# Kernel optimization log

Measured on AMD Instinct MI355X. Metric: run time of the kernel, lower is better.

The kernel has to match this reference:

```python
import jax, jax.numpy as jnp
import numpy as np

N_HEADS = 8


def setup_inputs() -> dict:
    key = jax.random.key(0)
    ks = jax.random.split(key, 12)
    B, C, H, W = 16, 256, 64, 64
    std = 1.0 / np.sqrt(C)  # init_std(conv) ~ 1/sqrt(fan_in) for a 1x1 conv
    return {
        "x": jax.random.normal(ks[0], (B, C, H, W), jnp.float32),
        "mod_multiplier": jax.random.normal(ks[1], (B, C), jnp.float32),
        "mod_bias": jax.random.normal(ks[2], (B, C), jnp.float32),
        "qkv_w": jax.random.normal(ks[3], (3 * C, C), jnp.float32) * std,
        "qkv_b": jnp.zeros((3 * C,), jnp.float32),
        "pe_q_h": jax.random.normal(ks[4], (1, C, H, 1), jnp.float32) * 0.02,
        "pe_q_w": jax.random.normal(ks[5], (1, C, 1, W), jnp.float32) * 0.02,
        "pe_k_h": jax.random.normal(ks[6], (1, C, H, 1), jnp.float32) * 0.02,
        "pe_k_w": jax.random.normal(ks[7], (1, C, 1, W), jnp.float32) * 0.02,
        "pre_act_bias": jnp.zeros((1, C, 1, 1), jnp.float32),
        "pre_qkv_bias": jnp.zeros((1, C, 1, 1), jnp.float32),
    }


def reference(x, mod_multiplier, mod_bias, qkv_w, qkv_b, pe_q_h, pe_q_w, pe_k_h, pe_k_w, pre_act_bias, pre_qkv_bias):
    B, C, H, W = x.shape
    hs = C // N_HEADS  # head_size
    dot_scale = jnp.asarray(hs, x.dtype) ** 0.5

    x_preact = jax.nn.silu(x + pre_act_bias)
    # 1x1 conv == channel GEMM: [B,C,H,W] x [3C,C] -> [B,3C,H,W]
    qkv = jnp.einsum('bchw,oc->bohw', x_preact + pre_qkv_bias, qkv_w) + qkv_b[None, :, None, None]
    q, k, v = jnp.split(qkv, 3, axis=1)

    q = q + pe_q_h + pe_q_w
    k = k + pe_k_h + pe_k_w
    q = q * mod_multiplier[:, :, None, None] + mod_bias[:, :, None, None]

    # view as [B, n_heads, head_size, H*W]
    q = q.reshape(B, N_HEADS, hs, H * W)
    k = k.reshape(B, N_HEADS, hs, H * W)
    v = v.reshape(B, N_HEADS, hs, H * W)

    # channel-attention: logits [B, n_heads, hs, hs]
    logits = jnp.einsum('bhcn,bhdn->bhcd', q, k) / dot_scale
    weights = jax.nn.softmax(logits, axis=-1)
    out = jnp.einsum('bhcd,bhdn->bhcn', weights, v).reshape(B, C, H, W)

    return jnp.concatenate((x_preact, out), axis=1)
```

## Files before the change

kernel.cpp:

```cpp
#include <hip/hip_runtime.h>

typedef short bf16x8 __attribute__((ext_vector_type(8)));
typedef float f32x4 __attribute__((ext_vector_type(4)));

__device__ __forceinline__ float b2f(unsigned short u) {
  union { unsigned int i; float f; } v; v.i = ((unsigned int)u) << 16; return v.f;
}
__device__ __forceinline__ unsigned short f2b(float f) {
  unsigned int u = __float_as_uint(f);
  u += 0x7fffu + ((u >> 16) & 1u);
  return (unsigned short)(u >> 16);
}
__device__ __forceinline__ float silu_f(float s) { return s / (1.0f + __expf(-s)); }

__device__ __forceinline__ void split2(float f, unsigned short& h, unsigned short& l) {
  h = f2b(f);
  l = f2b(f - b2f(h));
}

__device__ __forceinline__ void gload16(const unsigned short* g, unsigned short* l) {
  __builtin_amdgcn_global_load_lds(
      (const __attribute__((address_space(1))) unsigned int*)g,
      (__attribute__((address_space(3))) unsigned int*)l, 16, 0, 0);
}

__device__ __forceinline__ void unpack8(const unsigned* p, bf16x8& hi, bf16x8& lo) {
  uint4 a = *(const uint4*)p;
  uint4 b = *(const uint4*)(p + 4);
  unsigned u[8] = {a.x, a.y, a.z, a.w, b.x, b.y, b.z, b.w};
  unsigned hw[4], lw[4];
  #pragma unroll
  for (int j = 0; j < 4; j++) {
    hw[j] = __builtin_amdgcn_perm(u[2 * j + 1], u[2 * j], 0x05040100u);
    lw[j] = __builtin_amdgcn_perm(u[2 * j + 1], u[2 * j], 0x07060302u);
  }
  hi = *(bf16x8*)hw;
  lo = *(bf16x8*)lw;
}

__global__ __launch_bounds__(256) void k_prep(
    const float* __restrict__ x, const float* __restrict__ pab,
    const float* __restrict__ pqb, const float* __restrict__ W,
    unsigned short* __restrict__ Wfq, unsigned short* __restrict__ Wfl,
    unsigned short* __restrict__ Wfv, float* __restrict__ out) {
  __shared__ unsigned th2[64 * 32], tl2[64 * 32];
  int blk = blockIdx.x;
  if (blk < 96) {
    int u = blk * 256 + threadIdx.x;
    int lane = u & 63, l15 = lane & 15, l4 = lane >> 4;
    int row, k;
    unsigned short* dh;
    unsigned short* dl = nullptr;
    if (u < 16384) {
      int i = (u >> 6) & 3, step = (u >> 8) & 7, hh = u >> 11;
      row = (i < 2) ? (hh * 32 + i * 16 + l15) : (256 + hh * 32 + (i - 2) * 16 + l15);
      k = step * 32 + l4 * 8;
      dh = Wfq + (long long)u * 8;
      dl = Wfl + (long long)u * 8;
    } else {
      int u2 = u - 16384;
      int i2 = (u2 >> 6) & 1, step = (u2 >> 7) & 7, hh = u2 >> 10;
      row = 512 + hh * 32 + i2 * 16 + l15;
      k = step * 32 + l4 * 8;
      dh = Wfv + (long long)u2 * 8;
    }
    float4 a = *(const float4*)(W + row * 256 + k);
    float4 bq = *(const float4*)(W + row * 256 + k + 4);
    float v[8] = {a.x, a.y, a.z, a.w, bq.x, bq.y, bq.z, bq.w};
    unsigned short h8[8], l8[8];
    #pragma unroll
    for (int j = 0; j < 8; j++) split2(v[j], h8[j], l8[j]);
    uint4 ph;
    ph.x = h8[0] | ((unsigned)h8[1] << 16); ph.y = h8[2] | ((unsigned)h8[3] << 16);
    ph.z = h8[4] | ((unsigned)h8[5] << 16); ph.w = h8[6] | ((unsigned)h8[7] << 16);
    *(uint4*)dh = ph;
    if (dl) {
      uint4 pl;
      pl.x = l8[0] | ((unsigned)l8[1] << 16); pl.y = l8[2] | ((unsigned)l8[3] << 16);
      pl.z = l8[4] | ((unsigned)l8[5] << 16); pl.w = l8[6] | ((unsigned)l8[7] << 16);
      *(uint4*)dl = pl;
    }
    return;
  }
  blk -= 96;
  int nb = blk & 63;
  int cb = (blk >> 6) & 3;
  int b = blk >> 8;
  int n0 = nb * 64, c0 = cb * 64;
  int t = threadIdx.x;
  int nn = (t & 15) * 4;
  #pragma unroll
  for (int p = 0; p < 2; p++) {
    int cp = p * 16 + (t >> 4);
    int c = 2 * cp;
    float pa0 = pab[c0 + c], pq0 = pqb[c0 + c];
    float pa1 = pab[c0 + c + 1], pq1 = pqb[c0 + c + 1];
    float4 x0 = *(const float4*)(x + ((long long)(b * 256 + c0 + c)) * 4096 + n0 + nn);
    float4 x1 = *(const float4*)(x + ((long long)(b * 256 + c0 + c + 1)) * 4096 + n0 + nn);
    float s0[4] = {silu_f(x0.x + pa0), silu_f(x0.y + pa0),
                   silu_f(x0.z + pa0), silu_f(x0.w + pa0)};
    float s1[4] = {silu_f(x1.x + pa1), silu_f(x1.y + pa1),
                   silu_f(x1.z + pa1), silu_f(x1.w + pa1)};
    float4 sv0 = {s0[0], s0[1], s0[2], s0[3]};
    float4 sv1 = {s1[0], s1[1], s1[2], s1[3]};
    *(float4*)(out + ((long long)(b * 512 + c0 + c)) * 4096 + n0 + nn) = sv0;
    *(float4*)(out + ((long long)(b * 512 + c0 + c + 1)) * 4096 + n0 + nn) = sv1;
    float t0[4] = {s0[0] + pq0, s0[1] + pq0, s0[2] + pq0, s0[3] + pq0};
    float t1[4] = {s1[0] + pq1, s1[1] + pq1, s1[2] + pq1, s1[3] + pq1};
    #pragma unroll
    for (int j = 0; j < 4; j++) {
      int nr = nn + j;
      unsigned short h0, l0, h1, l1;
      split2(t0[j], h0, l0);
      split2(t1[j], h1, l1);
      int pidx = nr * 32 + (cp ^ (nr & 31));
      th2[pidx] = (unsigned)h0 | ((unsigned)h1 << 16);
      tl2[pidx] = (unsigned)l0 | ((unsigned)l1 << 16);
    }
  }
  __syncthreads();
  unsigned short* Th = (unsigned short*)(out + ((long long)(b * 512 + 256)) * 4096);
  unsigned short* Tl = Th + 4096 * 256;
  #pragma unroll
  for (int q = 0; q < 2; q++) {
    int s = q * 256 + t;
    int n = s >> 3, sc = s & 7;
    unsigned wh[4], wl[4];
    #pragma unroll
    for (int j = 0; j < 4; j++) {
      int pidx = n * 32 + ((sc * 4 + j) ^ (n & 31));
      wh[j] = th2[pidx];
      wl[j] = tl2[pidx];
    }
    uint4 vh = {wh[0], wh[1], wh[2], wh[3]};
    uint4 vl = {wl[0], wl[1], wl[2], wl[3]};
    *(uint4*)(Th + (long long)(n0 + n) * 256 + c0 + sc * 8) = vh;
    *(uint4*)(Tl + (long long)(n0 + n) * 256 + c0 + sc * 8) = vl;
  }
}

__global__ __launch_bounds__(256, 3) void k_qkl(
    const unsigned short* __restrict__ Wfq, const unsigned short* __restrict__ Wfl,
    const unsigned short* __restrict__ Wfv,
    const float* __restrict__ qkvb,
    const float* __restrict__ peqh, const float* __restrict__ peqw,
    const float* __restrict__ pekh, const float* __restrict__ pekw,
    const float* __restrict__ modm, const float* __restrict__ modb,
    const float* __restrict__ outT, float* __restrict__ kv,
    float* __restrict__ logits) {
  __shared__ __align__(16) unsigned char smem[33792];
  unsigned short* stg = (unsigned short*)smem;
  unsigned* qk = (unsigned*)smem;
  float* red = (float*)smem;

  int bx = blockIdx.x;
  int ntile = bx & 31, h = (bx >> 5) & 7, b = bx >> 8;
  int n0 = ntile * 128;
  int t = threadIdx.x, lane = t & 63, w = t >> 6;
  int l15 = lane & 15, l4 = lane >> 4;

  const unsigned short* Th =
      (const unsigned short*)(outT + ((long long)(b * 512 + 256)) * 4096);
  const unsigned short* Tl = Th + 4096 * 256;

  const unsigned short* csrc[4];
  unsigned short* cdst[4];
  int lrow = lane >> 2;
  int lslot = ((lane & 3) ^ ((lane >> 3) & 3)) * 8;
  #pragma unroll
  for (int i = 0; i < 4; i++) {
    int c = w + 4 * i;
    const unsigned short* plane = (c < 8) ? Th : Tl;
    int rowb = n0 + (c & 7) * 16;
    csrc[i] = plane + (long long)(rowb + lrow) * 256 + lslot;
    cdst[i] = stg + c * 512;
  }

  const unsigned short* aqb = Wfq + (long long)(h * 32) * 512 + lane * 8;
  const unsigned short* alb = Wfl + (long long)(h * 32) * 512 + lane * 8;
  const unsigned short* avb = Wfv + (long long)(h * 16) * 512 + lane * 8;

  int sw = (l4 ^ ((l15 >> 1) & 3)) << 3;
  f32x4 z = {0.f, 0.f, 0.f, 0.f};
  f32x4 acc[4][2];
  f32x4 accv[2][2];
  #pragma unroll
  for (int i = 0; i < 4; i++)
    #pragma unroll
    for (int j = 0; j < 2; j++) acc[i][j] = z;
  #pragma unroll
  for (int i = 0; i < 2; i++)
    #pragma unroll
    for (int j = 0; j < 2; j++) accv[i][j] = z;

  for (int step = 0; step < 8; ++step) {
    int k0 = step * 32;
    #pragma unroll
    for (int i = 0; i < 4; i++) gload16(csrc[i] + k0, cdst[i]);
    bf16x8 ah[4], alo[4], av[2];
    #pragma unroll
    for (int i = 0; i < 4; i++) {
      ah[i]  = *(const bf16x8*)(aqb + (step * 4 + i) * 512);
      alo[i] = *(const bf16x8*)(alb + (step * 4 + i) * 512);
    }
    #pragma unroll
    for (int i = 0; i < 2; i++)
      av[i] = *(const bf16x8*)(avb + (step * 2 + i) * 512);
    __syncthreads();
    bf16x8 bh[2], bl[2];
    #pragma unroll
    for (int j = 0; j < 2; j++) {
      int ro = (w * 32 + j * 16 + l15) * 32 + sw;
      bh[j] = *(const bf16x8*)(stg + ro);
      bl[j] = *(const bf16x8*)(stg + 4096 + ro);
    }
    #pragma unroll
    for (int i = 0; i < 2; i++)
      #pragma unroll
      for (int j = 0; j < 2; j++)
        accv[i][j] = __builtin_amdgcn_mfma_f32_16x16x32_bf16(av[i], bh[j], accv[i][j], 0, 0, 0);
    #pragma unroll
    for (int i = 0; i < 4; i++)
      #pragma unroll
      for (int j = 0; j < 2; j++) {
        acc[i][j] = __builtin_amdgcn_mfma_f32_16x16x32_bf16(ah[i], bh[j], acc[i][j], 0, 0, 0);
        acc[i][j] = __builtin_amdgcn_mfma_f32_16x16x32_bf16(ah[i], bl[j], acc[i][j], 0, 0, 0);
        acc[i][j] = __builtin_amdgcn_mfma_f32_16x16x32_bf16(alo[i], bh[j], acc[i][j], 0, 0, 0);
      }
    __syncthreads();
  }

  int b256 = b * 256;
  #pragma unroll
  for (int i = 0; i < 2; i++) {
    #pragma unroll
    for (int r = 0; r < 4; r++) {
      int row = i * 16 + l4 * 4 + r;
      int cch = h * 32 + row;
      float bias = qkvb[512 + cch];
      #pragma unroll
      for (int j = 0; j < 2; j++) {
        int n = n0 + w * 32 + j * 16 + l15;
        kv[((long long)(b256 + cch)) * 4096 + n] = accv[i][j][r] + bias;
      }
    }
  }

  #pragma unroll
  for (int i = 0; i < 4; i++) {
    #pragma unroll
    for (int r = 0; r < 4; r++) {
      int row = i * 16 + l4 * 4 + r;
      int cch = h * 32 + (row & 31);
      float bias = qkvb[(row & 32) ? (256 + cch) : cch];
      float mm = 0.f, mb = 0.f;
      if (row < 32) { mm = modm[b256 + cch]; mb = modb[b256 + cch]; }
      #pragma unroll
      for (int j = 0; j < 2; j++) {
        int nl = w * 32 + j * 16 + l15;
        int n = n0 + nl;
        int hh = n >> 6, ww = n & 63;
        float v = acc[i][j][r] + bias;
        if (row < 32) {
          v += peqh[cch * 64 + hh] + peqw[cch * 64 + ww];
          v = v * mm + mb;
        } else {
          v += pekh[cch * 64 + hh] + pekw[cch * 64 + ww];
        }
        unsigned short hi_, lo_;
        split2(v, hi_, lo_);
        int pch = (nl >> 3) ^ (row & 15);
        qk[row * 132 + pch * 8 + (nl & 7)] = (unsigned)hi_ | ((unsigned)lo_ << 16);
      }
    }
  }
  __syncthreads();

  f32x4 acc2[2][2] = {z, z, z, z};
  int chn = w * 4 + l4;
  bf16x8 qh[2], ql[2], kh[2], kl[2];
  #pragma unroll
  for (int i2 = 0; i2 < 2; i2++) {
    int row = i2 * 16 + l15;
    unpack8(qk + row * 132 + ((chn ^ l15) << 3), qh[i2], ql[i2]);
    unpack8(qk + (row + 32) * 132 + ((chn ^ l15) << 3), kh[i2], kl[i2]);
  }
  acc2[0][0] = __builtin_amdgcn_mfma_f32_16x16x32_bf16(qh[0], kh[0], acc2[0][0], 0, 0, 0);
  acc2[0][0] = __builtin_amdgcn_mfma_f32_16x16x32_bf16(qh[0], kl[0], acc2[0][0], 0, 0, 0);
  acc2[0][0] = __builtin_amdgcn_mfma_f32_16x16x32_bf16(ql[0], kh[0], acc2[0][0], 0, 0, 0);
  acc2[0][1] = __builtin_amdgcn_mfma_f32_16x16x32_bf16(qh[0], kh[1], acc2[0][1], 0, 0, 0);
  acc2[0][1] = __builtin_amdgcn_mfma_f32_16x16x32_bf16(qh[0], kl[1], acc2[0][1], 0, 0, 0);
  acc2[0][1] = __builtin_amdgcn_mfma_f32_16x16x32_bf16(ql[0], kh[1], acc2[0][1], 0, 0, 0);
  acc2[1][0] = __builtin_amdgcn_mfma_f32_16x16x32_bf16(qh[1], kh[0], acc2[1][0], 0, 0, 0);
  acc2[1][0] = __builtin_amdgcn_mfma_f32_16x16x32_bf16(qh[1], kl[0], acc2[1][0], 0, 0, 0);
  acc2[1][0] = __builtin_amdgcn_mfma_f32_16x16x32_bf16(ql[1], kh[0], acc2[1][0], 0, 0, 0);
  acc2[1][1] = __builtin_amdgcn_mfma_f32_16x16x32_bf16(qh[1], kh[1], acc2[1][1], 0, 0, 0);
  acc2[1][1] = __builtin_amdgcn_mfma_f32_16x16x32_bf16(qh[1], kl[1], acc2[1][1], 0, 0, 0);
  acc2[1][1] = __builtin_amdgcn_mfma_f32_16x16x32_bf16(ql[1], kh[1], acc2[1][1], 0, 0, 0);

  __syncthreads();
  #pragma unroll
  for (int i2 = 0; i2 < 2; i2++)
    #pragma unroll
    for (int j2 = 0; j2 < 2; j2++)
      #pragma unroll
      for (int r = 0; r < 4; r++)
        red[w * 1056 + (i2 * 16 + l4 * 4 + r) * 33 + j2 * 16 + l15] = acc2[i2][j2][r];
  __syncthreads();
  const float scale = 0.1767766952966369f;
  int bhid = b * 8 + h;
  #pragma unroll
  for (int i = 0; i < 4; i++) {
    int idx = i * 256 + t;
    int crow = idx >> 5, dcol = idx & 31;
    int ro = crow * 33 + dcol;
    float s = (red[ro] + red[1056 + ro] + red[2112 + ro] + red[3168 + ro]) * scale;
    atomicAdd(logits + (long long)bhid * 1024 + idx, s);
  }
}

__global__ __launch_bounds__(256) void k_pv(
    const float* __restrict__ kv,
    const float* __restrict__ logits,
    float* __restrict__ out) {
  int bx = blockIdx.x;
  int ntile = bx & 15, bh = bx >> 4;
  int b = bh >> 3, h = bh & 7;
  int t = threadIdx.x;
  __shared__ float raw[32][33];
  __shared__ float wsm[32][33];
  #pragma unroll
  for (int i = 0; i < 4; i++) {
    int idx = i * 256 + t;
    raw[idx >> 5][idx & 31] = logits[(long long)bh * 1024 + idx];
  }
  __syncthreads();
  if (t < 32) {
    float mx = -1e30f;
    for (int d = 0; d < 32; d++) mx = fmaxf(mx, raw[t][d]);
    float e[32]; float s = 0.f;
    for (int d = 0; d < 32; d++) { e[d] = __expf(raw[t][d] - mx); s += e[d]; }
    float inv = 1.0f / s;
    for (int d = 0; d < 32; d++) wsm[t][d] = e[d] * inv;
  }
  __syncthreads();
  int rg = t >> 6;
  int nl = (t & 63) * 4;
  int n0 = ntile * 256 + nl;
  const float* vb = kv + ((long long)(b * 256 + h * 32)) * 4096 + n0;
  float acc[8][4];
  #pragma unroll
  for (int r = 0; r < 8; r++)
    #pragma unroll
    for (int i = 0; i < 4; i++) acc[r][i] = 0.f;
  for (int d = 0; d < 32; d++) {
    float4 vv = *(const float4*)(vb + (long long)d * 4096);
    #pragma unroll
    for (int r = 0; r < 8; r++) {
      float wv = wsm[rg * 8 + r][d];
      acc[r][0] += wv * vv.x; acc[r][1] += wv * vv.y;
      acc[r][2] += wv * vv.z; acc[r][3] += wv * vv.w;
    }
  }
  #pragma unroll
  for (int r = 0; r < 8; r++) {
    long long oidx = ((long long)(b * 512 + 256 + h * 32 + rg * 8 + r)) * 4096 + n0;
    float4 ov = {acc[r][0], acc[r][1], acc[r][2], acc[r][3]};
    *(float4*)(out + oidx) = ov;
  }
}

extern "C" void kernel_launch(void* const* d_in, const int* in_sizes, int n_in,
                              void* d_out, int out_size, void* d_ws, size_t ws_size,
                              hipStream_t stream) {
  const float* x    = (const float*)d_in[0];
  const float* modm = (const float*)d_in[1];
  const float* modb = (const float*)d_in[2];
  const float* Wq   = (const float*)d_in[3];
  const float* qkvb = (const float*)d_in[4];
  const float* peqh = (const float*)d_in[5];
  const float* peqw = (const float*)d_in[6];
  const float* pekh = (const float*)d_in[7];
  const float* pekw = (const float*)d_in[8];
  const float* pab  = (const float*)d_in[9];
  const float* pqb  = (const float*)d_in[10];
  float* out = (float*)d_out;

  unsigned short* Wfq = (unsigned short*)d_ws;
  unsigned short* Wfl = Wfq + 131072;
  unsigned short* Wfv = Wfl + 131072;
  float* logits = (float*)((char*)d_ws + (1 << 20));
  float* kv = (float*)((char*)d_ws + 3 * (1 << 20));

  hipMemsetAsync(logits, 0, 16 * 8 * 32 * 32 * sizeof(float), stream);
  k_prep<<<4192, 256, 0, stream>>>(x, pab, pqb, Wq, Wfq, Wfl, Wfv, out);
  k_qkl<<<4096, 256, 0, stream>>>(Wfq, Wfl, Wfv, qkvb, peqh, peqw, pekh, pekw,
                                  modm, modb, out, kv, logits);
  k_pv<<<2048, 256, 0, stream>>>(kv, logits, out);
}
```

Before: 324.0 us.

## Fold softmax weights into V projection and compute output as GEMM on activations

Stops materializing V in fp32. Instead, softmax weights are multiplied into the V slice of the weight matrix in a small kernel (k_corr), producing an effective bf16 weight per batch/head plus a folded bias. A new double-buffered MFMA kernel (k_out) then computes the attention output directly from the split-bf16 activations. Weights are also staged through LDS in k_qkl instead of per-lane global loads, and the transposed activations now live in workspace rather than in the output buffer. This removes the kv write/read and the scalar PV kernel, at the cost of an extra launch and bf16-only precision on the folded weights.

Result: slower. 377.1 us (+16.4%).

```diff
diff --git a/kernel.cpp b/kernel.cpp
--- a/kernel.cpp
+++ b/kernel.cpp
@@ -41,48 +41,28 @@
 __global__ __launch_bounds__(256) void k_prep(
     const float* __restrict__ x, const float* __restrict__ pab,
     const float* __restrict__ pqb, const float* __restrict__ W,
-    unsigned short* __restrict__ Wfq, unsigned short* __restrict__ Wfl,
-    unsigned short* __restrict__ Wfv, float* __restrict__ out) {
+    unsigned short* __restrict__ Wh, unsigned short* __restrict__ Wl,
+    unsigned short* __restrict__ Tn, float* __restrict__ out) {
   __shared__ unsigned th2[64 * 32], tl2[64 * 32];
   int blk = blockIdx.x;
-  if (blk < 96) {
-    int u = blk * 256 + threadIdx.x;
-    int lane = u & 63, l15 = lane & 15, l4 = lane >> 4;
-    int row, k;
-    unsigned short* dh;
-    unsigned short* dl = nullptr;
-    if (u < 16384) {
-      int i = (u >> 6) & 3, step = (u >> 8) & 7, hh = u >> 11;
-      row = (i < 2) ? (hh * 32 + i * 16 + l15) : (256 + hh * 32 + (i - 2) * 16 + l15);
-      k = step * 32 + l4 * 8;
-      dh = Wfq + (long long)u * 8;
-      dl = Wfl + (long long)u * 8;
-    } else {
-      int u2 = u - 16384;
-      int i2 = (u2 >> 6) & 1, step = (u2 >> 7) & 7, hh = u2 >> 10;
-      row = 512 + hh * 32 + i2 * 16 + l15;
-      k = step * 32 + l4 * 8;
-      dh = Wfv + (long long)u2 * 8;
-    }
-    float4 a = *(const float4*)(W + row * 256 + k);
-    float4 bq = *(const float4*)(W + row * 256 + k + 4);
+  if (blk < 64) {
+    int e = (blk * 256 + threadIdx.x) * 8;
+    float4 a = *(const float4*)(W + e);
+    float4 bq = *(const float4*)(W + e + 4);
     float v[8] = {a.x, a.y, a.z, a.w, bq.x, bq.y, bq.z, bq.w};
     unsigned short h8[8], l8[8];
     #pragma unroll
     for (int j = 0; j < 8; j++) split2(v[j], h8[j], l8[j]);
-    uint4 ph;
+    uint4 ph, pl;
     ph.x = h8[0] | ((unsigned)h8[1] << 16); ph.y = h8[2] | ((unsigned)h8[3] << 16);
     ph.z = h8[4] | ((unsigned)h8[5] << 16); ph.w = h8[6] | ((unsigned)h8[7] << 16);
-    *(uint4*)dh = ph;
-    if (dl) {
-      uint4 pl;
-      pl.x = l8[0] | ((unsigned)l8[1] << 16); pl.y = l8[2] | ((unsigned)l8[3] << 16);
-      pl.z = l8[4] | ((unsigned)l8[5] << 16); pl.w = l8[6] | ((unsigned)l8[7] << 16);
-      *(uint4*)dl = pl;
-    }
+    pl.x = l8[0] | ((unsigned)l8[1] << 16); pl.y = l8[2] | ((unsigned)l8[3] << 16);
+    pl.z = l8[4] | ((unsigned)l8[5] << 16); pl.w = l8[6] | ((unsigned)l8[7] << 16);
+    *(uint4*)(Wh + e) = ph;
+    *(uint4*)(Wl + e) = pl;
     return;
   }
-  blk -= 96;
+  blk -= 64;
   int nb = blk & 63;
   int cb = (blk >> 6) & 3;
   int b = blk >> 8;
@@ -119,8 +99,8 @@
     }
   }
   __syncthreads();
-  unsigned short* Th = (unsigned short*)(out + ((long long)(b * 512 + 256)) * 4096);
-  unsigned short* Tl = Th + 4096 * 256;
+  unsigned short* Th = Tn + (long long)b * 2097152;
+  unsigned short* Tl = Th + 1048576;
   #pragma unroll
   for (int q = 0; q < 2; q++) {
     int s = q * 256 + t;
@@ -140,14 +120,12 @@
 }
 
 __global__ __launch_bounds__(256, 3) void k_qkl(
-    const unsigned short* __restrict__ Wfq, const unsigned short* __restrict__ Wfl,
-    const unsigned short* __restrict__ Wfv,
+    const unsigned short* __restrict__ Wh, const unsigned short* __restrict__ Wl,
     const float* __restrict__ qkvb,
     const float* __restrict__ peqh, const float* __restrict__ peqw,
     const float* __restrict__ pekh, const float* __restrict__ pekw,
     const float* __restrict__ modm, const float* __restrict__ modb,
-    const float* __restrict__ outT, float* __restrict__ kv,
-    float* __restrict__ logits) {
+    const unsigned short* __restrict__ Tn, float* __restrict__ logits) {
   __shared__ __align__(16) unsigned char smem[33792];
   unsigned short* stg = (unsigned short*)smem;
   unsigned* qk = (unsigned*)smem;
@@ -159,93 +137,70 @@
   int t = threadIdx.x, lane = t & 63, w = t >> 6;
   int l15 = lane & 15, l4 = lane >> 4;
 
-  const unsigned short* Th =
-      (const unsigned short*)(outT + ((long long)(b * 512 + 256)) * 4096);
-  const unsigned short* Tl = Th + 4096 * 256;
-
-  const unsigned short* csrc[4];
-  unsigned short* cdst[4];
+  const unsigned short* Thb = Tn + (long long)b * 2097152;
+  const unsigned short* Tlb = Thb + 1048576;
+
+  const unsigned short* csrc[6];
+  unsigned short* cdst[6];
   int lrow = lane >> 2;
   int lslot = ((lane & 3) ^ ((lane >> 3) & 3)) * 8;
   #pragma unroll
-  for (int i = 0; i < 4; i++) {
-    int c = w + 4 * i;
-    const unsigned short* plane = (c < 8) ? Th : Tl;
-    int rowb = n0 + (c & 7) * 16;
+  for (int i = 0; i < 6; i++) {
+    int c = w * 6 + i;
+    const unsigned short* plane;
+    int rowb;
+    if (c < 4) {
+      plane = Wh; rowb = ((c & 2) ? 256 : 0) + h * 32 + (c & 1) * 16;
+    } else if (c < 8) {
+      int s2 = c - 4;
+      plane = Wl; rowb = ((s2 & 2) ? 256 : 0) + h * 32 + (s2 & 1) * 16;
+    } else if (c < 16) {
+      plane = Thb; rowb = n0 + (c - 8) * 16;
+    } else {
+      plane = Tlb; rowb = n0 + (c - 16) * 16;
+    }
     csrc[i] = plane + (long long)(rowb + lrow) * 256 + lslot;
     cdst[i] = stg + c * 512;
   }
-
-  const unsigned short* aqb = Wfq + (long long)(h * 32) * 512 + lane * 8;
-  const unsigned short* alb = Wfl + (long long)(h * 32) * 512 + lane * 8;
-  const unsigned short* avb = Wfv + (long long)(h * 16) * 512 + lane * 8;
 
   int sw = (l4 ^ ((l15 >> 1) & 3)) << 3;
   f32x4 z = {0.f, 0.f, 0.f, 0.f};
   f32x4 acc[4][2];
-  f32x4 accv[2][2];
   #pragma unroll
   for (int i = 0; i < 4; i++)
     #pragma unroll
     for (int j = 0; j < 2; j++) acc[i][j] = z;
-  #pragma unroll
-  for (int i = 0; i < 2; i++)
-    #pragma unroll
-    for (int j = 0; j < 2; j++) accv[i][j] = z;
 
   for (int step = 0; step < 8; ++step) {
     int k0 = step * 32;
     #pragma unroll
-    for (int i = 0; i < 4; i++) gload16(csrc[i] + k0, cdst[i]);
-    bf16x8 ah[4], alo[4], av[2];
+    for (int i = 0; i < 6; i++) gload16(csrc[i] + k0, cdst[i]);
+    __syncthreads();
+    bf16x8 ah[4], al[4], bh[2], bl[2];
     #pragma unroll
     for (int i = 0; i < 4; i++) {
-      ah[i]  = *(const bf16x8*)(aqb + (step * 4 + i) * 512);
-      alo[i] = *(const bf16x8*)(alb + (step * 4 + i) * 512);
-    }
-    #pragma unroll
-    for (int i = 0; i < 2; i++)
-      av[i] = *(const bf16x8*)(avb + (step * 2 + i) * 512);
-    __syncthreads();
-    bf16x8 bh[2], bl[2];
+      int ro = (i * 16 + l15) * 32 + sw;
+      ah[i] = *(const bf16x8*)(stg + ro);
+      al[i] = *(const bf16x8*)(stg + 2048 + ro);
+    }
     #pragma unroll
     for (int j = 0; j < 2; j++) {
       int ro = (w * 32 + j * 16 + l15) * 32 + sw;
-      bh[j] = *(const bf16x8*)(stg + ro);
-      bl[j] = *(const bf16x8*)(stg + 4096 + ro);
-    }
-    #pragma unroll
-    for (int i = 0; i < 2; i++)
-      #pragma unroll
-      for (int j = 0; j < 2; j++)
-        accv[i][j] = __builtin_amdgcn_mfma_f32_16x16x32_bf16(av[i], bh[j], accv[i][j], 0, 0, 0);
+      bh[j] = *(const bf16x8*)(stg + 4096 + ro);
+      bl[j] = *(const bf16x8*)(stg + 8192 + ro);
+    }
     #pragma unroll
     for (int i = 0; i < 4; i++)
       #pragma unroll
       for (int j = 0; j < 2; j++) {
         acc[i][j] = __builtin_amdgcn_mfma_f32_16x16x32_bf16(ah[i], bh[j], acc[i][j], 0, 0, 0);
         acc[i][j] = __builtin_amdgcn_mfma_f32_16x16x32_bf16(ah[i], bl[j], acc[i][j], 0, 0, 0);
-        acc[i][j] = __builtin_amdgcn_mfma_f32_16x16x32_bf16(alo[i], bh[j], acc[i][j], 0, 0, 0);
+        acc[i][j] = __builtin_amdgcn_mfma_f32_16x16x32_bf16(al[i], bh[j], acc[i][j], 0, 0, 0);
       }
     __syncthreads();
   }
 
   int b256 = b * 256;
-  #pragma unroll
-  for (int i = 0; i < 2; i++) {
-    #pragma unroll
-    for (int r = 0; r < 4; r++) {
-      int row = i * 16 + l4 * 4 + r;
-      int cch = h * 32 + row;
-      float bias = qkvb[512 + cch];
-      #pragma unroll
-      for (int j = 0; j < 2; j++) {
-        int n = n0 + w * 32 + j * 16 + l15;
-        kv[((long long)(b256 + cch)) * 4096 + n] = accv[i][j][r] + bias;
-      }
-    }
-  }
-
   #pragma unroll
   for (int i = 0; i < 4; i++) {
     #pragma unroll
@@ -319,20 +274,19 @@
   }
 }
 
-__global__ __launch_bounds__(256) void k_pv(
-    const float* __restrict__ kv,
-    const float* __restrict__ logits,
-    float* __restrict__ out) {
+__global__ __launch_bounds__(256) void k_corr(
+    float* __restrict__ logits, const float* __restrict__ W,
+    const float* __restrict__ qkvb, unsigned short* __restrict__ Eh) {
   int bx = blockIdx.x;
-  int ntile = bx & 15, bh = bx >> 4;
-  int b = bh >> 3, h = bh & 7;
+  int b = bx >> 3, h = bx & 7;
   int t = threadIdx.x;
   __shared__ float raw[32][33];
   __shared__ float wsm[32][33];
+  long long lbase = (long long)bx * 1024;
   #pragma unroll
   for (int i = 0; i < 4; i++) {
     int idx = i * 256 + t;
-    raw[idx >> 5][idx & 31] = logits[(long long)bh * 1024 + idx];
+    raw[idx >> 5][idx & 31] = logits[lbase + idx];
   }
   __syncthreads();
   if (t < 32) {
@@ -344,29 +298,116 @@
     for (int d = 0; d < 32; d++) wsm[t][d] = e[d] * inv;
   }
   __syncthreads();
-  int rg = t >> 6;
-  int nl = (t & 63) * 4;
-  int n0 = ntile * 256 + nl;
-  const float* vb = kv + ((long long)(b * 256 + h * 32)) * 4096 + n0;
-  float acc[8][4];
-  #pragma unroll
-  for (int r = 0; r < 8; r++)
-    #pragma unroll
-    for (int i = 0; i < 4; i++) acc[r][i] = 0.f;
-  for (int d = 0; d < 32; d++) {
-    float4 vv = *(const float4*)(vb + (long long)d * 4096);
-    #pragma unroll
-    for (int r = 0; r < 8; r++) {
-      float wv = wsm[rg * 8 + r][d];
-      acc[r][0] += wv * vv.x; acc[r][1] += wv * vv.y;
-      acc[r][2] += wv * vv.z; acc[r][3] += wv * vv.w;
-    }
-  }
-  #pragma unroll
-  for (int r = 0; r < 8; r++) {
-    long long oidx = ((long long)(b * 512 + 256 + h * 32 + rg * 8 + r)) * 4096 + n0;
-    float4 ov = {acc[r][0], acc[r][1], acc[r][2], acc[r][3]};
-    *(float4*)(out + oidx) = ov;
+  if (t < 32) {
+    float s = 0.f;
+    for (int d = 0; d < 32; d++) s += wsm[t][d] * qkvb[512 + h * 32 + d];
+    logits[lbase + t] = s;
+  }
+  int r = t >> 3, e0 = (t & 7) * 32;
+  const float* WvB = W + (long long)(512 + h * 32) * 256;
+  unsigned* ebase = (unsigned*)(Eh + ((long long)(b * 256 + h * 32 + r)) * 256 + e0);
+  #pragma unroll 4
+  for (int eo = 0; eo < 32; eo += 2) {
+    float a0 = 0.f, a1 = 0.f;
+    for (int s = 0; s < 32; s++) {
+      float ws_ = wsm[r][s];
+      const float* wr = WvB + s * 256 + e0 + eo;
+      a0 += ws_ * wr[0];
+      a1 += ws_ * wr[1];
+    }
+    ebase[eo >> 1] = (unsigned)f2b(a0) | ((unsigned)f2b(a1) << 16);
+  }
+}
+
+__global__ __launch_bounds__(512, 4) void k_out(
+    const unsigned short* __restrict__ Eh, const unsigned short* __restrict__ Tn,
+    const float* __restrict__ logits,
+    float* __restrict__ out) {
+  extern __shared__ unsigned short sm[];
+  const int BUFS = 12288;
+  int bx = blockIdx.x;
+  int nt = bx & 31, mt = (bx >> 5) & 1, b = bx >> 6;
+  int n0 = nt * 128, m0 = mt * 128;
+  int t = threadIdx.x, lane = t & 63, w = t >> 6;
+  int wm = w >> 2, wn = w & 3;
+  int l15 = lane & 15, l4 = lane >> 4;
+  const unsigned short* Thb = Tn + (long long)b * 2097152;
+  const unsigned short* Tlb = Thb + 1048576;
+  const unsigned short* Ehb = Eh + (long long)b * 65536;
+
+  const unsigned short* csrc[3];
+  int dsto[3];
+  int lrow = lane >> 2;
+  int lslot = ((lane & 3) ^ ((lane >> 3) & 3)) * 8;
+  #pragma unroll
+  for (int i = 0; i < 3; i++) {
+    int c = w + 8 * i;
+    const unsigned short* plane = (c < 8) ? Ehb : ((c < 16) ? Thb : Tlb);
+    int rowb = (c < 8) ? (m0 + c * 16) : ((c < 16) ? (n0 + (c - 8) * 16)
+                                                   : (n0 + (c - 16) * 16));
+    csrc[i] = plane + (long long)(rowb + lrow) * 256 + lslot;
+    dsto[i] = c * 512;
+  }
+  int sw = (l4 ^ ((l15 >> 1) & 3)) << 3;
+
+  f32x4 z = {0.f, 0.f, 0.f, 0.f};
+  f32x4 acc[4][2];
+  #pragma unroll
+  for (int i = 0; i < 4; i++)
+    #pragma unroll
+    for (int j = 0; j < 2; j++) acc[i][j] = z;
+
+  #pragma unroll
+  for (int i = 0; i < 3; i++) gload16(csrc[i], sm + dsto[i]);
+
+  int cur = 0;
+  for (int step = 0; step < 8; ++step) {
+    if (step < 7) {
+      unsigned short* dp = sm + (cur ^ 1) * BUFS;
+      int k0 = (step + 1) * 32;
+      #pragma unroll
+      for (int i = 0; i < 3; i++) gload16(csrc[i] + k0, dp + dsto[i]);
+      asm volatile("s_waitcnt vmcnt(3)" ::: "memory");
+    } else {
+      asm volatile("s_waitcnt vmcnt(0)" ::: "memory");
+    }
+    __builtin_amdgcn_s_barrier();
+    __builtin_amdgcn_sched_barrier(0);
+    unsigned short* base = sm + cur * BUFS;
+    bf16x8 ah[4], bh[2], bl[2];
+    #pragma unroll
+    for (int i = 0; i < 4; i++)
+      ah[i] = *(const bf16x8*)(base + (wm * 64 + i * 16 + l15) * 32 + sw);
+    #pragma unroll
+    for (int j = 0; j < 2; j++) {
+      int ro = (wn * 32 + j * 16 + l15) * 32 + sw;
+      bh[j] = *(const bf16x8*)(base + 4096 + ro);
+      bl[j] = *(const bf16x8*)(base + 8192 + ro);
+    }
+    #pragma unroll
+    for (int i = 0; i < 4; i++)
+      #pragma unroll
+      for (int j = 0; j < 2; j++) {
+        acc[i][j] = __builtin_amdgcn_mfma_f32_16x16x32_bf16(ah[i], bh[j], acc[i][j], 0, 0, 0);
+        acc[i][j] = __builtin_amdgcn_mfma_f32_16x16x32_bf16(ah[i], bl[j], acc[i][j], 0, 0, 0);
+      }
+    __builtin_amdgcn_sched_barrier(0);
+    __builtin_amdgcn_s_barrier();
+    cur ^= 1;
+  }
+
+  #pragma unroll
+  for (int i = 0; i < 4; i++) {
+    #pragma unroll
+    for (int r = 0; r < 4; r++) {
+      int co = m0 + wm * 64 + i * 16 + l4 * 4 + r;
+      float be = logits[(long long)(b * 8 + (co >> 5)) * 1024 + (co & 31)];
+      #pragma unroll
+      for (int j = 0; j < 2; j++) {
+        int n = n0 + wn * 32 + j * 16 + l15;
+        out[((long long)(b * 512 + 256 + co)) * 4096 + n] = acc[i][j][r] + be;
+      }
+    }
   }
 }
 
@@ -386,15 +427,16 @@
   const float* pqb  = (const float*)d_in[10];
   float* out = (float*)d_out;
 
-  unsigned short* Wfq = (unsigned short*)d_ws;
-  unsigned short* Wfl = Wfq + 131072;
-  unsigned short* Wfv = Wfl + 131072;
-  float* logits = (float*)((char*)d_ws + (1 << 20));
-  float* kv = (float*)((char*)d_ws + 3 * (1 << 20));
-
-  hipMemsetAsync(logits, 0, 16 * 8 * 32 * 32 * sizeof(float), stream);
-  k_prep<<<4192, 256, 0, stream>>>(x, pab, pqb, Wq, Wfq, Wfl, Wfv, out);
-  k_qkl<<<4096, 256, 0, stream>>>(Wfq, Wfl, Wfv, qkvb, peqh, peqw, pekh, pekw,
-                                  modm, modb, out, kv, logits);
-  k_pv<<<2048, 256, 0, stream>>>(kv, logits, out);
-}
+  unsigned short* Tn = (unsigned short*)d_ws;
+  unsigned short* Wh = (unsigned short*)((char*)d_ws + 67108864);
+  unsigned short* Wl = Wh + 131072;
+  float* logits = (float*)((char*)d_ws + 67633152);
+  unsigned short* Eh = (unsigned short*)((char*)d_ws + 68157440);
+
+  hipMemsetAsync(logits, 0, 524288, stream);
+  k_prep<<<4160, 256, 0, stream>>>(x, pab, pqb, Wq, Wh, Wl, Tn, out);
+  k_qkl<<<4096, 256, 0, stream>>>(Wh, Wl, qkvb, peqh, peqw, pekh, pekw,
+                                  modm, modb, Tn, logits);
+  k_corr<<<128, 256, 0, stream>>>(logits, Wq, qkvb, Eh);
+  k_out<<<1024, 512, 49152, stream>>>(Eh, Tn, logits, out);
+}
```
